# Kernel tuning notes

Measured on AMD Instinct MI355X. Metric: run time of the kernel, lower is better.

## Reference

```python
import jax, jax.numpy as jnp
import numpy as np

TEMPERATURE = 0.05
MIN_SCALE = 0.01
MAX_SCALE = 1.0 - 0.001
EPS = 1e-7

N_NODES = 200000
N_LEAVES = 100000
RANK = 128
N_PAIRS = 1000000


def setup_inputs() -> dict:
    key = jax.random.key(0)
    k1, k2, k3, k4, k5, k6 = jax.random.split(key, 6)
    # internal-node embedding table (dumpy_node init, tiny norms as in init_size)
    embeddings_weight = jax.random.normal(k1, (N_NODES, RANK), dtype=jnp.float32) * 0.001
    # leaf embeddings: points strictly inside the Poincare ball
    u = jax.random.normal(k2, (N_LEAVES, RANK), dtype=jnp.float32)
    radii = jax.random.uniform(k3, (N_LEAVES, 1), minval=0.1, maxval=0.9, dtype=jnp.float32)
    leaves_embeddings = u / (jnp.linalg.norm(u, axis=1, keepdims=True) + 1e-6) * radii
    lca = jax.random.randint(k4, (1,), 0, N_NODES)
    l_idx = jax.random.randint(k5, (N_PAIRS,), 0, N_LEAVES)
    r_idx = jax.random.randint(k6, (N_PAIRS,), 0, N_LEAVES)
    sims = jax.random.uniform(jax.random.fold_in(key, 7), (N_PAIRS,), dtype=jnp.float32)
    scale = jnp.array([0.5], dtype=jnp.float32)
    return {"lca": lca, "l_idx": l_idx, "r_idx": r_idx, "sims": sims,
            "embeddings_weight": embeddings_weight,
            "leaves_embeddings": leaves_embeddings, "scale": scale}


def _hyp_dist(x, y):
    # Poincare-ball distance. x: [1, r], y: [P, r] -> [P]
    sq = jnp.sum((x - y) ** 2, axis=-1)
    nx = jnp.sum(x * x, axis=-1)
    ny = jnp.sum(y * y, axis=-1)
    arg = 1.0 + 2.0 * sq / ((1.0 - nx) * (1.0 - ny))
    return jnp.arccosh(jnp.clip(arg, 1.0 + EPS))


def reference(lca, l_idx, r_idx, sims, embeddings_weight, leaves_embeddings, scale):
    # embedding gather + L2-normalize * clamped scale
    e1 = embeddings_weight[lca]                             # [1, r]
    s = jnp.clip(scale, MIN_SCALE, MAX_SCALE)
    e1 = e1 / jnp.maximum(jnp.linalg.norm(e1, axis=1, keepdims=True), 1e-12) * s
    # vectorized hyperbolic pair distances (the original's Python loop)
    d = _hyp_dist(e1, leaves_embeddings[l_idx]) + _hyp_dist(e1, leaves_embeddings[r_idx])  # [P]
    weights = jax.nn.softmax(d / TEMPERATURE, axis=-1)
    w_ord = jnp.sum(sims * weights, axis=-1, keepdims=True)
    total = jnp.sum(sims, axis=-1, keepdims=True) - w_ord
    return jnp.mean(total)
```

## Files before the change

### kernel.cpp

```cpp
#include <hip/hip_runtime.h>
#include <math.h>

#define RANK 128
#define INV_T 20.0f
#define EPS_ARG 1e-7f
#define NBLK_PAIR 512

__global__ void k_prep(const float* __restrict__ emb, const int* __restrict__ lca,
                       const float* __restrict__ scale, float* __restrict__ e1ws) {
    __shared__ float wsum[2];
    __shared__ float bnorm;
    int i = threadIdx.x;
    int lane = i & 63, w = i >> 6;
    float v = emb[(size_t)lca[0] * RANK + i];
    float sq = v * v;
#pragma unroll
    for (int o = 32; o; o >>= 1) sq += __shfl_down(sq, o);
    if (lane == 0) wsum[w] = sq;
    __syncthreads();
    if (i == 0) bnorm = sqrtf(wsum[0] + wsum[1]);
    __syncthreads();
    float s = fminf(fmaxf(scale[0], 0.01f), 1.0f - 0.001f);
    float e1n = v / fmaxf(bnorm, 1e-12f) * s;
    e1ws[i] = e1n;
    float sq2 = e1n * e1n;
#pragma unroll
    for (int o = 32; o; o >>= 1) sq2 += __shfl_down(sq2, o);
    __syncthreads();
    if (lane == 0) wsum[w] = sq2;
    __syncthreads();
    if (i == 0) {
        float nx = wsum[0] + wsum[1];
        e1ws[RANK]     = nx;
        e1ws[RANK + 1] = 1.0f / (1.0f - nx);
    }
}

__global__ void k_leaf(const float4* __restrict__ leaves, const float* __restrict__ e1ws,
                       float* __restrict__ D, int nLeaves) {
    __shared__ float4 se1[RANK / 4];
    __shared__ float snx[2];
    int t = threadIdx.x;
    if (t < RANK / 4) se1[t] = ((const float4*)e1ws)[t];
    if (t == 0) { snx[0] = e1ws[RANK]; snx[1] = e1ws[RANK + 1]; }
    __syncthreads();
    int lane = t & 63, wid = t >> 6;
    int l31  = lane & 31, half = lane >> 5;
    int wavesPerBlock = blockDim.x >> 6;
    int gw = blockIdx.x * wavesPerBlock + wid;
    int nw = gridDim.x * wavesPerBlock;
    float nx = snx[0], invdx = snx[1];
    float4 e = se1[l31];
    for (int jj = gw; 2 * jj < nLeaves; jj += nw) {
        int j = 2 * jj + half;
        float dot = 0.0f, ny = 0.0f;
        if (j < nLeaves) {
            float4 y = leaves[(size_t)j * (RANK / 4) + l31];
            dot = y.x * e.x + y.y * e.y + y.z * e.z + y.w * e.w;
            ny  = y.x * y.x + y.y * y.y + y.z * y.z + y.w * y.w;
        }
#pragma unroll
        for (int o = 16; o; o >>= 1) {
            dot += __shfl_down(dot, o, 32);
            ny  += __shfl_down(ny, o, 32);
        }
        if (l31 == 0 && j < nLeaves) {
            float sq  = nx + ny - 2.0f * dot;
            float arg = 1.0f + 2.0f * sq * invdx / (1.0f - ny);
            arg = fmaxf(arg, 1.0f + EPS_ARG);
            D[j] = acoshf(arg);
        }
    }
}

__device__ inline void comb(float& m, float& z, float& w, float& s,
                            float m2, float z2, float w2, float s2) {
    float mn = fmaxf(m, m2);
    float a = (m  == mn) ? 1.0f : __expf(m  - mn);
    float b = (m2 == mn) ? 1.0f : __expf(m2 - mn);
    z = z * a + z2 * b;
    w = w * a + w2 * b;
    m = mn;
    s += s2;
}

__global__ void k_pair(const int* __restrict__ li, const int* __restrict__ ri,
                       const float* __restrict__ sims, const float* __restrict__ D,
                       float4* __restrict__ partials, int P) {
    float m = -INFINITY, z = 0.0f, w = 0.0f, s = 0.0f;
    int tid = blockIdx.x * blockDim.x + threadIdx.x;
    int nthreads = gridDim.x * blockDim.x;
    int P4 = P >> 2;
    const int4*   li4 = (const int4*)li;
    const int4*   ri4 = (const int4*)ri;
    const float4* s4p = (const float4*)sims;
    for (int i = tid; i < P4; i += nthreads) {
        int4 l = li4[i], r = ri4[i];
        float4 sv = s4p[i];
        float a0 = D[l.x], b0 = D[r.x];
        float a1 = D[l.y], b1 = D[r.y];
        float a2 = D[l.z], b2 = D[r.z];
        float a3 = D[l.w], b3 = D[r.w];
        float t0 = (a0 + b0) * INV_T, t1 = (a1 + b1) * INV_T;
        float t2 = (a2 + b2) * INV_T, t3 = (a3 + b3) * INV_T;
#define STEP(tp, svv)                                                  \
        if (tp <= m) { float e = __expf(tp - m); z += e; w = fmaf(svv, e, w); } \
        else { float rr = __expf(m - tp); z = fmaf(z, rr, 1.0f); w = fmaf(w, rr, svv); m = tp; } \
        s += svv;
        STEP(t0, sv.x) STEP(t1, sv.y) STEP(t2, sv.z) STEP(t3, sv.w)
    }
    int tail0 = P4 << 2;
    for (int p = tail0 + tid; p < P; p += nthreads) {
        float tp = (D[li[p]] + D[ri[p]]) * INV_T;
        float svv = sims[p];
        STEP(tp, svv)
    }
#undef STEP
#pragma unroll
    for (int o = 32; o; o >>= 1) {
        float m2 = __shfl_xor(m, o), z2 = __shfl_xor(z, o);
        float w2 = __shfl_xor(w, o), s2 = __shfl_xor(s, o);
        comb(m, z, w, s, m2, z2, w2, s2);
    }
    __shared__ float4 sp[8];
    int lane = threadIdx.x & 63, wid = threadIdx.x >> 6;
    if (lane == 0) sp[wid] = make_float4(m, z, w, s);
    __syncthreads();
    if (threadIdx.x == 0) {
        int nwv = blockDim.x >> 6;
        for (int i = 1; i < nwv; i++) {
            float4 q = sp[i];
            comb(m, z, w, s, q.x, q.y, q.z, q.w);
        }
        partials[blockIdx.x] = make_float4(m, z, w, s);
    }
}

__global__ void k_fin(const float4* __restrict__ partials, float* __restrict__ out, int nb) {
    int t = threadIdx.x;
    float m = -INFINITY, z = 0.0f, w = 0.0f, s = 0.0f;
    for (int i = t; i < nb; i += blockDim.x) {
        float4 q = partials[i];
        comb(m, z, w, s, q.x, q.y, q.z, q.w);
    }
#pragma unroll
    for (int o = 32; o; o >>= 1) {
        float m2 = __shfl_xor(m, o), z2 = __shfl_xor(z, o);
        float w2 = __shfl_xor(w, o), s2 = __shfl_xor(s, o);
        comb(m, z, w, s, m2, z2, w2, s2);
    }
    __shared__ float4 sp[4];
    int lane = t & 63, wid = t >> 6;
    if (lane == 0) sp[wid] = make_float4(m, z, w, s);
    __syncthreads();
    if (t == 0) {
        for (int i = 1; i < (int)(blockDim.x >> 6); i++) {
            float4 q = sp[i];
            comb(m, z, w, s, q.x, q.y, q.z, q.w);
        }
        out[0] = s - w / z;
    }
}

extern "C" void kernel_launch(void* const* d_in, const int* in_sizes, int n_in,
                              void* d_out, int out_size, void* d_ws, size_t ws_size,
                              hipStream_t stream) {
    const int*   lca    = (const int*)d_in[0];
    const int*   li     = (const int*)d_in[1];
    const int*   ri     = (const int*)d_in[2];
    const float* sims   = (const float*)d_in[3];
    const float* emb    = (const float*)d_in[4];
    const float* leaves = (const float*)d_in[5];
    const float* scale  = (const float*)d_in[6];
    float* out = (float*)d_out;

    int P       = in_sizes[1];
    int nLeaves = in_sizes[5] / RANK;

    char* ws = (char*)d_ws;
    float* e1ws = (float*)ws;
    float* D    = (float*)(ws + 1024);
    size_t poff = 1024 + (((size_t)nLeaves * sizeof(float) + 1023) / 1024) * 1024;
    float4* partials = (float4*)(ws + poff);

    k_prep<<<1, 128, 0, stream>>>(emb, lca, scale, e1ws);
    k_leaf<<<2048, 256, 0, stream>>>((const float4*)leaves, e1ws, D, nLeaves);
    k_pair<<<NBLK_PAIR, 256, 0, stream>>>(li, ri, sims, D, partials, P);
    k_fin <<<1, 256, 0, stream>>>(partials, out, NBLK_PAIR);
}
```

Measured before the change: 198.3 us.

## Fuse prep, leaf, pair and final kernels into one cooperative kernel

```diff
diff --git a/kernel.cpp b/kernel.cpp
--- a/kernel.cpp
+++ b/kernel.cpp
@@ -1,77 +1,14 @@
 #include <hip/hip_runtime.h>
+#include <hip/hip_cooperative_groups.h>
 #include <math.h>
+
+namespace cg = cooperative_groups;
 
 #define RANK 128
 #define INV_T 20.0f
 #define EPS_ARG 1e-7f
-#define NBLK_PAIR 512
-
-__global__ void k_prep(const float* __restrict__ emb, const int* __restrict__ lca,
-                       const float* __restrict__ scale, float* __restrict__ e1ws) {
-    __shared__ float wsum[2];
-    __shared__ float bnorm;
-    int i = threadIdx.x;
-    int lane = i & 63, w = i >> 6;
-    float v = emb[(size_t)lca[0] * RANK + i];
-    float sq = v * v;
-#pragma unroll
-    for (int o = 32; o; o >>= 1) sq += __shfl_down(sq, o);
-    if (lane == 0) wsum[w] = sq;
-    __syncthreads();
-    if (i == 0) bnorm = sqrtf(wsum[0] + wsum[1]);
-    __syncthreads();
-    float s = fminf(fmaxf(scale[0], 0.01f), 1.0f - 0.001f);
-    float e1n = v / fmaxf(bnorm, 1e-12f) * s;
-    e1ws[i] = e1n;
-    float sq2 = e1n * e1n;
-#pragma unroll
-    for (int o = 32; o; o >>= 1) sq2 += __shfl_down(sq2, o);
-    __syncthreads();
-    if (lane == 0) wsum[w] = sq2;
-    __syncthreads();
-    if (i == 0) {
-        float nx = wsum[0] + wsum[1];
-        e1ws[RANK]     = nx;
-        e1ws[RANK + 1] = 1.0f / (1.0f - nx);
-    }
-}
-
-__global__ void k_leaf(const float4* __restrict__ leaves, const float* __restrict__ e1ws,
-                       float* __restrict__ D, int nLeaves) {
-    __shared__ float4 se1[RANK / 4];
-    __shared__ float snx[2];
-    int t = threadIdx.x;
-    if (t < RANK / 4) se1[t] = ((const float4*)e1ws)[t];
-    if (t == 0) { snx[0] = e1ws[RANK]; snx[1] = e1ws[RANK + 1]; }
-    __syncthreads();
-    int lane = t & 63, wid = t >> 6;
-    int l31  = lane & 31, half = lane >> 5;
-    int wavesPerBlock = blockDim.x >> 6;
-    int gw = blockIdx.x * wavesPerBlock + wid;
-    int nw = gridDim.x * wavesPerBlock;
-    float nx = snx[0], invdx = snx[1];
-    float4 e = se1[l31];
-    for (int jj = gw; 2 * jj < nLeaves; jj += nw) {
-        int j = 2 * jj + half;
-        float dot = 0.0f, ny = 0.0f;
-        if (j < nLeaves) {
-            float4 y = leaves[(size_t)j * (RANK / 4) + l31];
-            dot = y.x * e.x + y.y * e.y + y.z * e.z + y.w * e.w;
-            ny  = y.x * y.x + y.y * y.y + y.z * y.z + y.w * y.w;
-        }
-#pragma unroll
-        for (int o = 16; o; o >>= 1) {
-            dot += __shfl_down(dot, o, 32);
-            ny  += __shfl_down(ny, o, 32);
-        }
-        if (l31 == 0 && j < nLeaves) {
-            float sq  = nx + ny - 2.0f * dot;
-            float arg = 1.0f + 2.0f * sq * invdx / (1.0f - ny);
-            arg = fmaxf(arg, 1.0f + EPS_ARG);
-            D[j] = acoshf(arg);
-        }
-    }
-}
+#define NBLK 512
+#define NTHR 256
 
 __device__ inline void comb(float& m, float& z, float& w, float& s,
                             float m2, float z2, float w2, float s2) {
@@ -84,81 +21,147 @@
     s += s2;
 }
 
-__global__ void k_pair(const int* __restrict__ li, const int* __restrict__ ri,
-                       const float* __restrict__ sims, const float* __restrict__ D,
-                       float4* __restrict__ partials, int P) {
-    float m = -INFINITY, z = 0.0f, w = 0.0f, s = 0.0f;
-    int tid = blockIdx.x * blockDim.x + threadIdx.x;
-    int nthreads = gridDim.x * blockDim.x;
-    int P4 = P >> 2;
-    const int4*   li4 = (const int4*)li;
-    const int4*   ri4 = (const int4*)ri;
-    const float4* s4p = (const float4*)sims;
-    for (int i = tid; i < P4; i += nthreads) {
-        int4 l = li4[i], r = ri4[i];
-        float4 sv = s4p[i];
-        float a0 = D[l.x], b0 = D[r.x];
-        float a1 = D[l.y], b1 = D[r.y];
-        float a2 = D[l.z], b2 = D[r.z];
-        float a3 = D[l.w], b3 = D[r.w];
-        float t0 = (a0 + b0) * INV_T, t1 = (a1 + b1) * INV_T;
-        float t2 = (a2 + b2) * INV_T, t3 = (a3 + b3) * INV_T;
+__global__ void k_fused(const int* __restrict__ lca,
+                        const int* __restrict__ li, const int* __restrict__ ri,
+                        const float* __restrict__ sims,
+                        const float* __restrict__ emb,
+                        const float4* __restrict__ leaves,
+                        const float* __restrict__ scale,
+                        float* D, float4* partials, float* out,
+                        int P, int nLeaves) {
+    cg::grid_group grid = cg::this_grid();
+
+    __shared__ float4 se1[RANK / 4];
+    __shared__ float  snx[2];
+    __shared__ float4 sp[NTHR / 64];
+
+    int t = threadIdx.x;
+
+    if (t < 32) {
+        float4 v = ((const float4*)(emb + (size_t)lca[0] * RANK))[t];
+        float sq = v.x * v.x + v.y * v.y + v.z * v.z + v.w * v.w;
+#pragma unroll
+        for (int o = 16; o; o >>= 1) sq += __shfl_down(sq, o, 32);
+        sq = __shfl(sq, 0, 32);
+        float bn = sqrtf(sq);
+        float s = fminf(fmaxf(scale[0], 0.01f), 1.0f - 0.001f);
+        float k = s / fmaxf(bn, 1e-12f);
+        float4 e; e.x = v.x * k; e.y = v.y * k; e.z = v.z * k; e.w = v.w * k;
+        se1[t] = e;
+        float sq2 = e.x * e.x + e.y * e.y + e.z * e.z + e.w * e.w;
+#pragma unroll
+        for (int o = 16; o; o >>= 1) sq2 += __shfl_down(sq2, o, 32);
+        if (t == 0) {
+            snx[0] = sq2;
+            snx[1] = 1.0f / (1.0f - sq2);
+        }
+    }
+    __syncthreads();
+
+    {
+        int lane = t & 63, wid = t >> 6;
+        int l31 = lane & 31, half = lane >> 5;
+        int wavesPerBlock = NTHR >> 6;
+        int gw = blockIdx.x * wavesPerBlock + wid;
+        int nw = gridDim.x * wavesPerBlock;
+        float nx = snx[0], invdx = snx[1];
+        float4 e = se1[l31];
+        for (int jj = gw; 2 * jj < nLeaves; jj += nw) {
+            int j = 2 * jj + half;
+            float dot = 0.0f, ny = 0.0f;
+            if (j < nLeaves) {
+                float4 y = leaves[(size_t)j * (RANK / 4) + l31];
+                dot = y.x * e.x + y.y * e.y + y.z * e.z + y.w * e.w;
+                ny  = y.x * y.x + y.y * y.y + y.z * y.z + y.w * y.w;
+            }
+#pragma unroll
+            for (int o = 16; o; o >>= 1) {
+                dot += __shfl_down(dot, o, 32);
+                ny  += __shfl_down(ny, o, 32);
+            }
+            if (l31 == 0 && j < nLeaves) {
+                float sq  = nx + ny - 2.0f * dot;
+                float arg = 1.0f + 2.0f * sq * invdx / (1.0f - ny);
+                arg = fmaxf(arg, 1.0f + EPS_ARG);
+                D[j] = acoshf(arg);
+            }
+        }
+    }
+    __threadfence();
+    grid.sync();
+
+    {
+        float m = -INFINITY, z = 0.0f, w = 0.0f, s = 0.0f;
+        int tid = blockIdx.x * NTHR + t;
+        int nthreads = gridDim.x * NTHR;
+        int P4 = P >> 2;
+        const int4*   li4 = (const int4*)li;
+        const int4*   ri4 = (const int4*)ri;
+        const float4* s4p = (const float4*)sims;
+        for (int i = tid; i < P4; i += nthreads) {
+            int4 l = li4[i], r = ri4[i];
+            float4 sv = s4p[i];
+            float a0 = D[l.x], b0 = D[r.x];
+            float a1 = D[l.y], b1 = D[r.y];
+            float a2 = D[l.z], b2 = D[r.z];
+            float a3 = D[l.w], b3 = D[r.w];
+            float t0 = (a0 + b0) * INV_T, t1 = (a1 + b1) * INV_T;
+            float t2 = (a2 + b2) * INV_T, t3 = (a3 + b3) * INV_T;
 #define STEP(tp, svv)                                                  \
-        if (tp <= m) { float e = __expf(tp - m); z += e; w = fmaf(svv, e, w); } \
-        else { float rr = __expf(m - tp); z = fmaf(z, rr, 1.0f); w = fmaf(w, rr, svv); m = tp; } \
-        s += svv;
-        STEP(t0, sv.x) STEP(t1, sv.y) STEP(t2, sv.z) STEP(t3, sv.w)
-    }
-    int tail0 = P4 << 2;
-    for (int p = tail0 + tid; p < P; p += nthreads) {
-        float tp = (D[li[p]] + D[ri[p]]) * INV_T;
-        float svv = sims[p];
-        STEP(tp, svv)
-    }
+            if (tp <= m) { float e = __expf(tp - m); z += e; w = fmaf(svv, e, w); } \
+            else { float rr = __expf(m - tp); z = fmaf(z, rr, 1.0f); w = fmaf(w, rr, svv); m = tp; } \
+            s += svv;
+            STEP(t0, sv.x) STEP(t1, sv.y) STEP(t2, sv.z) STEP(t3, sv.w)
+        }
+        int tail0 = P4 << 2;
+        for (int p = tail0 + tid; p < P; p += nthreads) {
+            float tp = (D[li[p]] + D[ri[p]]) * INV_T;
+            float svv = sims[p];
+            STEP(tp, svv)
+        }
 #undef STEP
 #pragma unroll
-    for (int o = 32; o; o >>= 1) {
-        float m2 = __shfl_xor(m, o), z2 = __shfl_xor(z, o);
-        float w2 = __shfl_xor(w, o), s2 = __shfl_xor(s, o);
-        comb(m, z, w, s, m2, z2, w2, s2);
+        for (int o = 32; o; o >>= 1) {
+            float m2 = __shfl_xor(m, o), z2 = __shfl_xor(z, o);
+            float w2 = __shfl_xor(w, o), s2 = __shfl_xor(s, o);
+            comb(m, z, w, s, m2, z2, w2, s2);
+        }
+        int lane = t & 63, wid = t >> 6;
+        if (lane == 0) sp[wid] = make_float4(m, z, w, s);
+        __syncthreads();
+        if (t == 0) {
+            for (int i = 1; i < (NTHR >> 6); i++) {
+                float4 q = sp[i];
+                comb(m, z, w, s, q.x, q.y, q.z, q.w);
+            }
+            partials[blockIdx.x] = make_float4(m, z, w, s);
+        }
     }
-    __shared__ float4 sp[8];
-    int lane = threadIdx.x & 63, wid = threadIdx.x >> 6;
-    if (lane == 0) sp[wid] = make_float4(m, z, w, s);
-    __syncthreads();
-    if (threadIdx.x == 0) {
-        int nwv = blockDim.x >> 6;
-        for (int i = 1; i < nwv; i++) {
-            float4 q = sp[i];
+    __threadfence();
+    grid.sync();
+
+    if (blockIdx.x == 0) {
+        float m = -INFINITY, z = 0.0f, w = 0.0f, s = 0.0f;
+        for (int i = t; i < NBLK; i += NTHR) {
+            float4 q = partials[i];
             comb(m, z, w, s, q.x, q.y, q.z, q.w);
         }
-        partials[blockIdx.x] = make_float4(m, z, w, s);
-    }
-}
-
-__global__ void k_fin(const float4* __restrict__ partials, float* __restrict__ out, int nb) {
-    int t = threadIdx.x;
-    float m = -INFINITY, z = 0.0f, w = 0.0f, s = 0.0f;
-    for (int i = t; i < nb; i += blockDim.x) {
-        float4 q = partials[i];
-        comb(m, z, w, s, q.x, q.y, q.z, q.w);
-    }
 #pragma unroll
-    for (int o = 32; o; o >>= 1) {
-        float m2 = __shfl_xor(m, o), z2 = __shfl_xor(z, o);
-        float w2 = __shfl_xor(w, o), s2 = __shfl_xor(s, o);
-        comb(m, z, w, s, m2, z2, w2, s2);
-    }
-    __shared__ float4 sp[4];
-    int lane = t & 63, wid = t >> 6;
-    if (lane == 0) sp[wid] = make_float4(m, z, w, s);
-    __syncthreads();
-    if (t == 0) {
-        for (int i = 1; i < (int)(blockDim.x >> 6); i++) {
-            float4 q = sp[i];
-            comb(m, z, w, s, q.x, q.y, q.z, q.w);
+        for (int o = 32; o; o >>= 1) {
+            float m2 = __shfl_xor(m, o), z2 = __shfl_xor(z, o);
+            float w2 = __shfl_xor(w, o), s2 = __shfl_xor(s, o);
+            comb(m, z, w, s, m2, z2, w2, s2);
         }
-        out[0] = s - w / z;
+        int lane = t & 63, wid = t >> 6;
+        if (lane == 0) sp[wid] = make_float4(m, z, w, s);
+        __syncthreads();
+        if (t == 0) {
+            for (int i = 1; i < (NTHR >> 6); i++) {
+                float4 q = sp[i];
+                comb(m, z, w, s, q.x, q.y, q.z, q.w);
+            }
+            out[0] = s - w / z;
+        }
     }
 }
 
@@ -178,13 +181,16 @@
     int nLeaves = in_sizes[5] / RANK;
 
     char* ws = (char*)d_ws;
-    float* e1ws = (float*)ws;
-    float* D    = (float*)(ws + 1024);
-    size_t poff = 1024 + (((size_t)nLeaves * sizeof(float) + 1023) / 1024) * 1024;
+    float*  D        = (float*)ws;
+    size_t  poff     = (((size_t)nLeaves * sizeof(float) + 1023) / 1024) * 1024;
     float4* partials = (float4*)(ws + poff);
 
-    k_prep<<<1, 128, 0, stream>>>(emb, lca, scale, e1ws);
-    k_leaf<<<2048, 256, 0, stream>>>((const float4*)leaves, e1ws, D, nLeaves);
-    k_pair<<<NBLK_PAIR, 256, 0, stream>>>(li, ri, sims, D, partials, P);
-    k_fin <<<1, 256, 0, stream>>>(partials, out, NBLK_PAIR);
+    const float4* leaves4 = (const float4*)leaves;
+    void* args[] = {
+        (void*)&lca, (void*)&li, (void*)&ri, (void*)&sims, (void*)&emb,
+        (void*)&leaves4, (void*)&scale, (void*)&D, (void*)&partials,
+        (void*)&out, (void*)&P, (void*)&nLeaves
+    };
+    hipLaunchCooperativeKernel(reinterpret_cast<void*>(k_fused),
+                               dim3(NBLK), dim3(NTHR), args, 0, stream);
 }
```

Result: slower. 446.3 us (+125.1%).
